# Kernel optimization log

Measured on AMD Instinct MI355X. Metric: run time of the kernel, lower is better.

The kernel has to match this reference:

```python
import jax, jax.numpy as jnp
import numpy as np

BT, C, H, W = 16, 64, 128, 128
K, S = 16, 8            # ksize, stride2
MID = C // 2            # BasicBlock mid channels
INTER = C // 1          # r = 1 -> inter_channels = channels
NH = (H - K) // S + 1
NW = (W - K) // S + 1
L = NH * NW             # 225 patches


def _lrelu(x):
    return jnp.where(x > 0, x, 0.2 * x)


def _conv(x, w):
    return jax.lax.conv_general_dilated(
        x, w, window_strides=(1, 1), padding='VALID',
        dimension_numbers=('NCHW', 'OIHW', 'NCHW'))


def setup_inputs() -> dict:
    key = jax.random.key(0)
    ks = jax.random.split(key, 7)
    fea = jax.random.normal(ks[0], (BT, C, H, W), jnp.float32)
    spa_graph = jax.random.normal(ks[1], (BT, L, L), jnp.float32) * 0.05
    spe_graph = jax.random.normal(ks[2], (BT, C, C), jnp.float32) * 0.05
    W1 = jax.random.normal(ks[3], (MID, C, 3, 3), jnp.float32) * 0.05
    W2 = jax.random.normal(ks[4], (C, MID, 1, 1), jnp.float32) * 0.05
    Wl = jax.random.normal(ks[5], (INTER, C, 1, 1), jnp.float32) * 0.05
    bl = jnp.zeros((INTER,), jnp.float32)
    return {'fea': fea, 'spa_graph': spa_graph, 'spe_graph': spe_graph,
            'W1': W1, 'W2': W2, 'Wl': Wl, 'bl': bl}


def reference(fea, spa_graph, spe_graph, W1, W2, Wl, bl):
    bt, c, h, w = fea.shape
    # BasicBlock: reflect-pad conv3x3 -> lrelu -> conv1x1 -> lrelu
    xp = jnp.pad(fea, ((0, 0), (0, 0), (1, 1), (1, 1)), mode='reflect')
    f = _lrelu(_conv(_lrelu(_conv(xp, W1)), W2))            # [bt,c,h,w]

    # unfold (torch.nn.Unfold order: (C, kh, kw) feature-major, row-major patches)
    patches = jax.lax.conv_general_dilated_patches(f, (K, K), (S, S), 'VALID')
    cols = patches.reshape(bt, c * K * K, L)                 # [bt,F,L]

    # per-sample spatial-graph matmul: graph[p,q] @ patches[q,F]
    out_spa = jnp.einsum('bpq,bfq->bfp', spa_graph, cols)    # [bt,F,L]

    # fold: overlap-add patches back to [bt,c,h,w]
    rows = jnp.arange(NH) * S + jnp.arange(K)[:, None]       # [K,NH]
    colsi = jnp.arange(NW) * S + jnp.arange(K)[:, None]      # [K,NW]
    lin = (rows[:, None, :, None] * w + colsi[None, :, None, :]).reshape(-1)
    vals = out_spa.reshape(bt, c, K * K * L)
    x = jnp.zeros((bt, c, h * w), fea.dtype).at[:, :, lin].add(vals)
    x = x.reshape(bt, c, h, w)

    # per-sample spectral-graph matmul
    residual = jnp.einsum('bcd,bdn->bcn', spe_graph,
                          f.reshape(bt, c, h * w)).reshape(bt, c, h, w)

    xa = 0.5 * (x + residual)
    xl = _lrelu(_conv(xa, Wl) + bl[None, :, None, None])
    wei = jax.nn.sigmoid(xl)
    return x * wei + residual * (1.0 - wei) + f
```

## Files before the change

kernel.cpp:

```cpp
#include <hip/hip_runtime.h>
#include <hip/hip_bf16.h>
#include <hip/hip_runtime_api.h>

#define BT 16
#define CCH 64
#define H 128
#define W 128
#define STR 8
#define NH 15
#define NW 15
#define L 225
#define HW (H * W)

#define UPITCH 264
#define CP 72
#define MP 40

typedef __attribute__((ext_vector_type(8))) short short8;
typedef __attribute__((ext_vector_type(4))) float f32x4;
typedef __attribute__((ext_vector_type(4))) unsigned short ushort4_t;

__device__ __forceinline__ float lrelu(float v) { return v > 0.f ? v : 0.2f * v; }
__device__ __forceinline__ unsigned short f2bf(float v) {
  __hip_bfloat16 h = __float2bfloat16(v);
  unsigned short u;
  __builtin_memcpy(&u, &h, 2);
  return u;
}
__device__ __forceinline__ float bf2f(unsigned short u) {
  unsigned int x = ((unsigned int)u) << 16;
  float f;
  __builtin_memcpy(&f, &x, 4);
  return f;
}

__global__ __launch_bounds__(256) void prep_w_k(
    const float* __restrict__ W1, const float* __restrict__ W2,
    const float* __restrict__ spe, const float* __restrict__ Wl,
    __hip_bfloat16* __restrict__ W1r, __hip_bfloat16* __restrict__ W2r,
    __hip_bfloat16* __restrict__ spe_r, __hip_bfloat16* __restrict__ wl_r) {
  const int idx = blockIdx.x * 256 + threadIdx.x;
  if (idx < 18432) {
    const int kk = idx >> 10, mc = (idx >> 5) & 31, ck = idx & 31;
    const int pos = kk >> 1, s = kk & 1;
    W1r[idx] = __float2bfloat16(W1[(mc * 64 + s * 32 + ck) * 9 + pos]);
    return;
  }
  int i = idx - 18432;
  if (i < 2048) { W2r[i] = __float2bfloat16(W2[i]); return; }
  i -= 2048;
  if (i < BT * CCH * CCH) { spe_r[i] = __float2bfloat16(spe[i]); return; }
  i -= BT * CCH * CCH;
  if (i < CCH * CCH) { wl_r[i] = __float2bfloat16(Wl[i]); return; }
}

__global__ __launch_bounds__(256) void fea_t_k(
    const float* __restrict__ fea, __hip_bfloat16* __restrict__ ft) {
  const int b = blockIdx.y;
  const int p0 = blockIdx.x * 256;
  const int tid = threadIdx.x;
#pragma unroll 1
  for (int it = 0; it < 8; ++it) {
    const int u = it * 256 + tid;
    const int px = u >> 3, g = u & 7;
    const int p = p0 + px;
    short8 v;
#pragma unroll
    for (int j = 0; j < 8; ++j)
      v[j] = (short)f2bf(fea[((size_t)b * CCH + g * 8 + j) * HW + p]);
    *(short8*)&ft[((size_t)b * HW + p) * CCH + g * 8] = v;
  }
}

__global__ __launch_bounds__(256) void spa_comb_k(
    const float* __restrict__ spa, __hip_bfloat16* __restrict__ T) {
  const int bp = blockIdx.x;
  const int b = bp >> 8, pi = bp & 255;
  const int k = threadIdx.x;
  const int yi = pi >> 4, xi = pi & 15;
  const int ky = k >> 4, kx = k & 15;
  const float* sb = spa + (size_t)b * L * L;
  float acc = 0.f;
#pragma unroll
  for (int vy = 0; vy < 2; ++vy)
#pragma unroll
    for (int vx = 0; vx < 2; ++vx) {
      const int py = yi - vy, px = xi - vx;
      const int qy = ky - vy, qx = kx - vx;
      if (py >= 0 && py < NH && px >= 0 && px < NW && qy >= 0 && qy < NH &&
          qx >= 0 && qx < NW)
        acc += sb[(py * NW + px) * L + qy * NW + qx];
    }
  T[(size_t)bp * 256 + k] = __float2bfloat16(acc);
}

__global__ __launch_bounds__(512) void bblock_mfma_k(
    const __hip_bfloat16* __restrict__ ft, const __hip_bfloat16* __restrict__ W1r,
    const __hip_bfloat16* __restrict__ W2r, __hip_bfloat16* __restrict__ fnh) {
  __shared__ __align__(16) short st[324 * CP];
  __shared__ __align__(16) short mids[256 * MP];
  const int b = blockIdx.z, ty0 = blockIdx.y * 16, tx0 = blockIdx.x * 16;
  const int tid = threadIdx.x;

  for (int i = tid; i < 2592; i += 512) {
    const int px = i >> 3, g = i & 7;
    const int iy = px / 18, ix = px - iy * 18;
    int gy = ty0 + iy - 1;
    gy = gy < 0 ? -gy : (gy > 127 ? 254 - gy : gy);
    int gx = tx0 + ix - 1;
    gx = gx < 0 ? -gx : (gx > 127 ? 254 - gx : gx);
    *(short8*)&st[px * CP + g * 8] =
        *(const short8*)&ft[((size_t)b * HW + gy * W + gx) * CCH + g * 8];
  }
  __syncthreads();

  const int w = tid >> 6, lane = tid & 63, lm = lane & 15, lk = lane >> 4;
  const short* w1 = (const short*)W1r;
  const short* w2 = (const short*)W2r;

  f32x4 acc[2][2];
#pragma unroll
  for (int mt = 0; mt < 2; ++mt)
#pragma unroll
    for (int t = 0; t < 2; ++t) acc[mt][t] = (f32x4){0.f, 0.f, 0.f, 0.f};

#pragma unroll
  for (int pos = 0; pos < 9; ++pos) {
    const int dy = pos / 3, dx = pos - dy * 3;
#pragma unroll
    for (int s = 0; s < 2; ++s) {
      short8 a0 = *(const short8*)&w1[((pos * 2 + s) * 32 + lm) * 32 + lk * 8];
      short8 a1 = *(const short8*)&w1[((pos * 2 + s) * 32 + 16 + lm) * 32 + lk * 8];
#pragma unroll
      for (int t = 0; t < 2; ++t) {
        const int p = (w * 2 + t + dy) * 18 + lm + dx;
        short8 bb = *(const short8*)&st[p * CP + s * 32 + lk * 8];
        acc[0][t] = __builtin_amdgcn_mfma_f32_16x16x32_bf16(a0, bb, acc[0][t], 0, 0, 0);
        acc[1][t] = __builtin_amdgcn_mfma_f32_16x16x32_bf16(a1, bb, acc[1][t], 0, 0, 0);
      }
    }
  }

#pragma unroll
  for (int t = 0; t < 2; ++t) {
    const int n = (w * 2 + t) * 16 + lm;
#pragma unroll
    for (int mt = 0; mt < 2; ++mt) {
      ushort4_t pk;
#pragma unroll
      for (int r = 0; r < 4; ++r) pk[r] = f2bf(lrelu(acc[mt][t][r]));
      *(ushort4_t*)&mids[n * MP + mt * 16 + lk * 4] = pk;
    }
  }
  __syncthreads();

  f32x4 acc2[4][2];
#pragma unroll
  for (int m2 = 0; m2 < 4; ++m2)
#pragma unroll
    for (int t = 0; t < 2; ++t) acc2[m2][t] = (f32x4){0.f, 0.f, 0.f, 0.f};

  short8 b2[2];
#pragma unroll
  for (int t = 0; t < 2; ++t)
    b2[t] = *(const short8*)&mids[((w * 2 + t) * 16 + lm) * MP + lk * 8];
#pragma unroll
  for (int m2 = 0; m2 < 4; ++m2) {
    short8 a2 = *(const short8*)&w2[(m2 * 16 + lm) * 32 + lk * 8];
#pragma unroll
    for (int t = 0; t < 2; ++t)
      acc2[m2][t] = __builtin_amdgcn_mfma_f32_16x16x32_bf16(a2, b2[t], acc2[m2][t], 0, 0, 0);
  }

  unsigned short* fo = (unsigned short*)fnh;
#pragma unroll
  for (int m2 = 0; m2 < 4; ++m2)
#pragma unroll
    for (int t = 0; t < 2; ++t) {
      const int y = ty0 + w * 2 + t, x = tx0 + lm;
      ushort4_t pk;
#pragma unroll
      for (int r = 0; r < 4; ++r) pk[r] = f2bf(lrelu(acc2[m2][t][r]));
      *(ushort4_t*)&fo[((size_t)b * HW + y * W + x) * CCH + m2 * 16 + lk * 4] = pk;
    }
}

__global__ __launch_bounds__(512) void spa_mfma_k(
    const __hip_bfloat16* __restrict__ fnh, const __hip_bfloat16* __restrict__ T,
    __hip_bfloat16* __restrict__ xnh) {
  __shared__ __align__(16) short us[CCH * UPITCH];

  const int lb = ((int)blockIdx.x % 8) * 128 + (int)blockIdx.x / 8;
  const int b = lb >> 6, ky0 = (lb >> 3) & 7, kx0 = lb & 7;
  const int tid = threadIdx.x;

  const unsigned short* fb = (const unsigned short*)fnh + (size_t)b * HW * CCH;

  for (int i = tid; i < 2048; i += 512) {
    const int pos = i >> 3, g = i & 7;
    const int gy = pos >> 4, gx = pos & 15;
    const int blk = pos >> 3;
    short8 v = *(const short8*)&fb[((ky0 + 8 * gy) * W + kx0 + 8 * gx) * CCH + g * 8];
#pragma unroll
    for (int e = 0; e < 8; ++e) {
      const int c = g * 8 + e;
      const int sblk = (blk & ~7) | ((blk ^ (c >> 3)) & 7);
      us[c * UPITCH + sblk * 8 + (pos & 7)] = v[e];
    }
  }
  __syncthreads();

  const int w = tid >> 6, lane = tid & 63;
  const int lm = lane & 15, lk = lane >> 4;
  const int mtg = w >> 2, ntg = w & 3;

  const short* tb = (const short*)T + (size_t)b * 256 * 256;

  f32x4 acc[2][4];
#pragma unroll
  for (int mt = 0; mt < 2; ++mt)
#pragma unroll
    for (int n = 0; n < 4; ++n) acc[mt][n] = (f32x4){0.f, 0.f, 0.f, 0.f};

  const int c0 = (mtg * 2) * 16 + lm, c1 = (mtg * 2 + 1) * 16 + lm;

#pragma unroll
  for (int k8 = 0; k8 < 8; ++k8) {
    const int kb = k8 * 4 + lk;
    const int sb0 = (kb & ~7) | ((kb ^ (c0 >> 3)) & 7);
    const int sb1 = (kb & ~7) | ((kb ^ (c1 >> 3)) & 7);
    short8 a0 = *(const short8*)&us[c0 * UPITCH + sb0 * 8];
    short8 a1 = *(const short8*)&us[c1 * UPITCH + sb1 * 8];
    short8 bb[4];
#pragma unroll
    for (int n = 0; n < 4; ++n)
      bb[n] = *(const short8*)&tb[((ntg * 4 + n) * 16 + lm) * 256 + k8 * 32 + lk * 8];
#pragma unroll
    for (int n = 0; n < 4; ++n) {
      acc[0][n] = __builtin_amdgcn_mfma_f32_16x16x32_bf16(a0, bb[n], acc[0][n], 0, 0, 0);
      acc[1][n] = __builtin_amdgcn_mfma_f32_16x16x32_bf16(a1, bb[n], acc[1][n], 0, 0, 0);
    }
  }

  unsigned short* xo = (unsigned short*)xnh + (size_t)b * HW * CCH;
#pragma unroll
  for (int mt = 0; mt < 2; ++mt)
#pragma unroll
    for (int n = 0; n < 4; ++n) {
      const int row = (ntg * 4 + n) * 8 + ky0;
      const int col = lm * 8 + kx0;
      ushort4_t pk;
#pragma unroll
      for (int r = 0; r < 4; ++r) pk[r] = f2bf(acc[mt][n][r]);
      *(ushort4_t*)&xo[((size_t)row * W + col) * CCH + (mtg * 2 + mt) * 16 + lk * 4] = pk;
    }
}

__global__ __launch_bounds__(256) void final_mfma_k(
    const __hip_bfloat16* __restrict__ fnh, const __hip_bfloat16* __restrict__ xnh,
    const __hip_bfloat16* __restrict__ spe_r, const __hip_bfloat16* __restrict__ wl_r,
    const float* __restrict__ bl, float* __restrict__ xo) {
  __shared__ __align__(16) short fl[128 * CP];
  __shared__ __align__(16) short xal[128 * CP];
  const int b = blockIdx.y;
  const int px0 = blockIdx.x * 128;
  const int tid = threadIdx.x;

  for (int i = tid; i < 128 * 8; i += 256) {
    const int px = i >> 3, g = i & 7;
    *(short8*)&fl[px * CP + g * 8] =
        *(const short8*)&fnh[((size_t)b * HW + px0 + px) * CCH + g * 8];
  }
  __syncthreads();

  const int w = tid >> 6, lane = tid & 63, lm = lane & 15, lk = lane >> 4;
  const int c0 = w * 16 + lk * 4;

  const short* sa = (const short*)spe_r + ((size_t)b * CCH + w * 16 + lm) * CCH;
  const short8 a1_0 = *(const short8*)&sa[lk * 8];
  const short8 a1_1 = *(const short8*)&sa[32 + lk * 8];

  const unsigned short* xb = (const unsigned short*)xnh + (size_t)b * HW * CCH;

  f32x4 res[8];
  f32x4 xar[8];
#pragma unroll
  for (int nt = 0; nt < 8; ++nt) {
    const int prow = (nt * 16 + lm) * CP;
    short8 b0 = *(const short8*)&fl[prow + lk * 8];
    short8 b1 = *(const short8*)&fl[prow + 32 + lk * 8];
    f32x4 r = (f32x4){0.f, 0.f, 0.f, 0.f};
    r = __builtin_amdgcn_mfma_f32_16x16x32_bf16(a1_0, b0, r, 0, 0, 0);
    r = __builtin_amdgcn_mfma_f32_16x16x32_bf16(a1_1, b1, r, 0, 0, 0);
    res[nt] = r;
    ushort4_t xq = *(const ushort4_t*)&xb[(size_t)(px0 + nt * 16 + lm) * CCH + c0];
    ushort4_t pk;
    f32x4 xa;
#pragma unroll
    for (int j = 0; j < 4; ++j) {
      xa[j] = 0.5f * (bf2f(xq[j]) + r[j]);
      pk[j] = f2bf(xa[j]);
    }
    xar[nt] = xa;
    *(ushort4_t*)&xal[(nt * 16 + lm) * CP + c0] = pk;
  }
  __syncthreads();

  const short* wa = (const short*)wl_r + (w * 16 + lm) * CCH;
  const short8 a2_0 = *(const short8*)&wa[lk * 8];
  const short8 a2_1 = *(const short8*)&wa[32 + lk * 8];
  float blv[4];
#pragma unroll
  for (int j = 0; j < 4; ++j) blv[j] = bl[c0 + j];

#pragma unroll
  for (int nt = 0; nt < 8; ++nt) {
    const int prow = (nt * 16 + lm) * CP;
    short8 b0 = *(const short8*)&xal[prow + lk * 8];
    short8 b1 = *(const short8*)&xal[prow + 32 + lk * 8];
    f32x4 t = (f32x4){0.f, 0.f, 0.f, 0.f};
    t = __builtin_amdgcn_mfma_f32_16x16x32_bf16(a2_0, b0, t, 0, 0, 0);
    t = __builtin_amdgcn_mfma_f32_16x16x32_bf16(a2_1, b1, t, 0, 0, 0);
    ushort4_t fpk = *(const ushort4_t*)&fl[prow + c0];
#pragma unroll
    for (int j = 0; j < 4; ++j) {
      const float xl = lrelu(t[j] + blv[j]);
      const float wei = 1.f / (1.f + __expf(-xl));
      const float o = 2.f * xar[nt][j] * wei + res[nt][j] * (1.f - 2.f * wei) +
                      bf2f(fpk[j]);
      xo[((size_t)b * CCH + c0 + j) * HW + px0 + nt * 16 + lm] = o;
    }
  }
}

extern "C" void kernel_launch(void* const* d_in, const int* in_sizes, int n_in,
                              void* d_out, int out_size, void* d_ws,
                              size_t ws_size, hipStream_t stream) {
  const float* fea = (const float*)d_in[0];
  const float* spa = (const float*)d_in[1];
  const float* spe = (const float*)d_in[2];
  const float* W1  = (const float*)d_in[3];
  const float* W2  = (const float*)d_in[4];
  const float* Wl  = (const float*)d_in[5];
  const float* bl  = (const float*)d_in[6];
  float* out = (float*)d_out;

  const size_t FT_BYTES  = (size_t)BT * HW * CCH * 2;
  const size_t FNH_BYTES = (size_t)BT * HW * CCH * 2;
  const size_t T_BYTES   = (size_t)BT * 256 * 256 * 2;
  char* wsb = (char*)d_ws;
  __hip_bfloat16* ft  = (__hip_bfloat16*)wsb;
  __hip_bfloat16* xnh = (__hip_bfloat16*)wsb;
  __hip_bfloat16* fnh = (__hip_bfloat16*)(wsb + FT_BYTES);
  __hip_bfloat16* T   = (__hip_bfloat16*)(wsb + FT_BYTES + FNH_BYTES);
  char* wtb = wsb + FT_BYTES + FNH_BYTES + T_BYTES;
  __hip_bfloat16* W1r   = (__hip_bfloat16*)wtb;
  __hip_bfloat16* W2r   = (__hip_bfloat16*)(wtb + 36864);
  __hip_bfloat16* spe_r = (__hip_bfloat16*)(wtb + 36864 + 4096);
  __hip_bfloat16* wl_r  = (__hip_bfloat16*)(wtb + 36864 + 4096 + 131072);

  prep_w_k<<<dim3(352), 256, 0, stream>>>(W1, W2, spe, Wl, W1r, W2r, spe_r, wl_r);
  fea_t_k<<<dim3(HW / 256, BT), 256, 0, stream>>>(fea, ft);
  spa_comb_k<<<dim3(BT * 256), 256, 0, stream>>>(spa, T);
  bblock_mfma_k<<<dim3(8, 8, BT), 512, 0, stream>>>(ft, W1r, W2r, fnh);
  spa_mfma_k<<<dim3(BT * 64), 512, 0, stream>>>(fnh, T, xnh);
  final_mfma_k<<<dim3(HW / 128, BT), 256, 0, stream>>>(fnh, xnh, spe_r, wl_r, bl, out);
}
```

Measured before the change: 138.0 us.

## Merge prep kernels, alias bblock LDS buffers, and swizzle block order across XCDs

Folds the weight-prep, feature-transpose and spatial-graph combine kernels into one launch, which removes two kernel launches and their inter-kernel gaps. The bblock kernel now reuses the staging LDS buffer for the mid activations, with an extra barrier between the two uses, to cut shared memory per block and allow more resident blocks. Block indices in the prep, bblock and final kernels are remapped so that consecutive tiles of a sample land on the same XCD, aiming for better L2 locality. The risks are the extra barrier and a single large heterogeneous launch whose differently sized work parts may balance poorly.

```diff
diff --git a/kernel.cpp b/kernel.cpp
--- a/kernel.cpp
+++ b/kernel.cpp
@@ -34,12 +34,57 @@
   return f;
 }
 
-__global__ __launch_bounds__(256) void prep_w_k(
+__global__ __launch_bounds__(256) void prep_all_k(
+    const float* __restrict__ fea, const float* __restrict__ spa,
     const float* __restrict__ W1, const float* __restrict__ W2,
     const float* __restrict__ spe, const float* __restrict__ Wl,
+    __hip_bfloat16* __restrict__ ft, __hip_bfloat16* __restrict__ T,
     __hip_bfloat16* __restrict__ W1r, __hip_bfloat16* __restrict__ W2r,
     __hip_bfloat16* __restrict__ spe_r, __hip_bfloat16* __restrict__ wl_r) {
-  const int idx = blockIdx.x * 256 + threadIdx.x;
+  const int bid = blockIdx.x;
+  const int tid = threadIdx.x;
+
+  if (bid < 1024) {
+    const int lb = (bid % 8) * 128 + bid / 8;
+    const int b = lb >> 6;
+    const int p0 = (lb & 63) * 256;
+#pragma unroll 1
+    for (int it = 0; it < 8; ++it) {
+      const int u = it * 256 + tid;
+      const int px = u >> 3, g = u & 7;
+      const int p = p0 + px;
+      short8 v;
+#pragma unroll
+      for (int j = 0; j < 8; ++j)
+        v[j] = (short)f2bf(fea[((size_t)b * CCH + g * 8 + j) * HW + p]);
+      *(short8*)&ft[((size_t)b * HW + p) * CCH + g * 8] = v;
+    }
+    return;
+  }
+
+  if (bid < 5120) {
+    const int bp = bid - 1024;
+    const int b = bp >> 8, pi = bp & 255;
+    const int k = tid;
+    const int yi = pi >> 4, xi = pi & 15;
+    const int ky = k >> 4, kx = k & 15;
+    const float* sb = spa + (size_t)b * L * L;
+    float acc = 0.f;
+#pragma unroll
+    for (int vy = 0; vy < 2; ++vy)
+#pragma unroll
+      for (int vx = 0; vx < 2; ++vx) {
+        const int py = yi - vy, px = xi - vx;
+        const int qy = ky - vy, qx = kx - vx;
+        if (py >= 0 && py < NH && px >= 0 && px < NW && qy >= 0 && qy < NH &&
+            qx >= 0 && qx < NW)
+          acc += sb[(py * NW + px) * L + qy * NW + qx];
+      }
+    T[(size_t)bp * 256 + k] = __float2bfloat16(acc);
+    return;
+  }
+
+  const int idx = (bid - 5120) * 256 + tid;
   if (idx < 18432) {
     const int kk = idx >> 10, mc = (idx >> 5) & 31, ck = idx & 31;
     const int pos = kk >> 1, s = kk & 1;
@@ -54,52 +99,17 @@
   if (i < CCH * CCH) { wl_r[i] = __float2bfloat16(Wl[i]); return; }
 }
 
-__global__ __launch_bounds__(256) void fea_t_k(
-    const float* __restrict__ fea, __hip_bfloat16* __restrict__ ft) {
-  const int b = blockIdx.y;
-  const int p0 = blockIdx.x * 256;
-  const int tid = threadIdx.x;
-#pragma unroll 1
-  for (int it = 0; it < 8; ++it) {
-    const int u = it * 256 + tid;
-    const int px = u >> 3, g = u & 7;
-    const int p = p0 + px;
-    short8 v;
-#pragma unroll
-    for (int j = 0; j < 8; ++j)
-      v[j] = (short)f2bf(fea[((size_t)b * CCH + g * 8 + j) * HW + p]);
-    *(short8*)&ft[((size_t)b * HW + p) * CCH + g * 8] = v;
-  }
-}
-
-__global__ __launch_bounds__(256) void spa_comb_k(
-    const float* __restrict__ spa, __hip_bfloat16* __restrict__ T) {
-  const int bp = blockIdx.x;
-  const int b = bp >> 8, pi = bp & 255;
-  const int k = threadIdx.x;
-  const int yi = pi >> 4, xi = pi & 15;
-  const int ky = k >> 4, kx = k & 15;
-  const float* sb = spa + (size_t)b * L * L;
-  float acc = 0.f;
-#pragma unroll
-  for (int vy = 0; vy < 2; ++vy)
-#pragma unroll
-    for (int vx = 0; vx < 2; ++vx) {
-      const int py = yi - vy, px = xi - vx;
-      const int qy = ky - vy, qx = kx - vx;
-      if (py >= 0 && py < NH && px >= 0 && px < NW && qy >= 0 && qy < NH &&
-          qx >= 0 && qx < NW)
-        acc += sb[(py * NW + px) * L + qy * NW + qx];
-    }
-  T[(size_t)bp * 256 + k] = __float2bfloat16(acc);
-}
-
 __global__ __launch_bounds__(512) void bblock_mfma_k(
     const __hip_bfloat16* __restrict__ ft, const __hip_bfloat16* __restrict__ W1r,
     const __hip_bfloat16* __restrict__ W2r, __hip_bfloat16* __restrict__ fnh) {
-  __shared__ __align__(16) short st[324 * CP];
-  __shared__ __align__(16) short mids[256 * MP];
-  const int b = blockIdx.z, ty0 = blockIdx.y * 16, tx0 = blockIdx.x * 16;
+  __shared__ __align__(16) short sbuf[324 * CP];
+  short* st = sbuf;
+  short* mids = sbuf;
+
+  const int lb = ((int)blockIdx.x % 8) * 128 + (int)blockIdx.x / 8;
+  const int b = lb >> 6;
+  const int tile = lb & 63;
+  const int ty0 = (tile >> 3) * 16, tx0 = (tile & 7) * 16;
   const int tid = threadIdx.x;
 
   for (int i = tid; i < 2592; i += 512) {
@@ -141,6 +151,8 @@
     }
   }
 
+  __syncthreads();
+
 #pragma unroll
   for (int t = 0; t < 2; ++t) {
     const int n = (w * 2 + t) * 16 + lm;
@@ -262,8 +274,9 @@
     const float* __restrict__ bl, float* __restrict__ xo) {
   __shared__ __align__(16) short fl[128 * CP];
   __shared__ __align__(16) short xal[128 * CP];
-  const int b = blockIdx.y;
-  const int px0 = blockIdx.x * 128;
+  const int lb = ((int)blockIdx.x % 8) * 256 + (int)blockIdx.x / 8;
+  const int b = lb >> 7;
+  const int px0 = (lb & 127) * 128;
   const int tid = threadIdx.x;
 
   for (int i = tid; i < 128 * 8; i += 256) {
@@ -359,10 +372,9 @@
   __hip_bfloat16* spe_r = (__hip_bfloat16*)(wtb + 36864 + 4096);
   __hip_bfloat16* wl_r  = (__hip_bfloat16*)(wtb + 36864 + 4096 + 131072);
 
-  prep_w_k<<<dim3(352), 256, 0, stream>>>(W1, W2, spe, Wl, W1r, W2r, spe_r, wl_r);
-  fea_t_k<<<dim3(HW / 256, BT), 256, 0, stream>>>(fea, ft);
-  spa_comb_k<<<dim3(BT * 256), 256, 0, stream>>>(spa, T);
-  bblock_mfma_k<<<dim3(8, 8, BT), 512, 0, stream>>>(ft, W1r, W2r, fnh);
+  prep_all_k<<<dim3(5472), 256, 0, stream>>>(fea, spa, W1, W2, spe, Wl,
+                                             ft, T, W1r, W2r, spe_r, wl_r);
+  bblock_mfma_k<<<dim3(1024), 512, 0, stream>>>(ft, W1r, W2r, fnh);
   spa_mfma_k<<<dim3(BT * 64), 512, 0, stream>>>(fnh, T, xnh);
-  final_mfma_k<<<dim3(HW / 128, BT), 256, 0, stream>>>(fnh, xnh, spe_r, wl_r, bl, out);
-}
+  final_mfma_k<<<dim3(2048), 256, 0, stream>>>(fnh, xnh, spe_r, wl_r, bl, out);
+}
```

Result: faster. 133.0 us (-3.7%).
